# Performance work log

Measured on AMD Instinct MI355X. Metric: run time of the kernel, lower is better.

Reference implementation:

```python
import jax, jax.numpy as jnp
import numpy as np

H = 16         # heads
DH = 64        # dim_head
IMG = 32       # image_size (axial axis=0, along height)
SEQ_LEN = 1279 # seq_len
DIM = 1024
SCALE = DH ** -0.5


def setup_inputs() -> dict:
    key = jax.random.key(0)
    k1, k2, k3 = jax.random.split(key, 3)
    x = jax.random.normal(k1, (16, SEQ_LEN, DIM), dtype=jnp.float32)
    w_qkv = jax.random.normal(k2, (3 * H * DH, DIM), dtype=jnp.float32) * 0.02
    w_out = jax.random.normal(k3, (DIM, H * DH), dtype=jnp.float32) * 0.02
    b_out = jnp.zeros((DIM,), dtype=jnp.float32)
    return {"x": x, "w_qkv": w_qkv, "w_out": w_out, "b_out": b_out}


def reference(x, w_qkv, w_out, b_out):
    b, n, _ = x.shape
    img_seq = IMG * IMG                  # 1024
    text_len = SEQ_LEN + 1 - img_seq     # 256
    padding = SEQ_LEN - n + 1
    xp = jnp.pad(x, ((0, 0), (0, padding), (0, 0)))  # [b, seq_len+1, dim]

    qkv = xp @ w_qkv.T                   # [b, N, 3*H*DH]
    q, k, v = jnp.split(qkv, 3, axis=-1)

    def to_heads(t):
        B, N, _ = t.shape
        return t.reshape(B, N, H, DH).transpose(0, 2, 1, 3).reshape(B * H, N, DH)

    q, k, v = map(to_heads, (q, k, v))   # [(b h), N, DH]
    q = q * SCALE

    q_t, q_i = q[:, :-img_seq], q[:, -img_seq:]
    k_t, k_i = k[:, :-img_seq], k[:, -img_seq:]
    v_t, v_i = v[:, :-img_seq], v[:, -img_seq:]

    # ---- text self-attention (causal) ----
    dots_text = jnp.einsum('bid,bjd->bij', q_t, k_t)  # [(b h), T, T]
    mask_value = -jnp.finfo(dots_text.dtype).max
    T = text_len
    text_causal = jnp.triu(jnp.ones((T, T), dtype=bool), 1)
    dots_text = jnp.where(text_causal[None], mask_value, dots_text)
    attn_text = jax.nn.softmax(dots_text, axis=-1)
    out_text = jnp.einsum('bij,bjd->bid', attn_text, v_t)  # [(b h), T, DH]

    # ---- axial image attention (axis=0: attend along width within each row) ----
    qi = q_i.reshape(b * H, IMG, IMG, DH)  # b (h w) d -> b h w d
    ki = k_i.reshape(b * H, IMG, IMG, DH)
    vi = v_i.reshape(b * H, IMG, IMG, DH)

    dots_ii = jnp.einsum('bxid,bxjd->bxij', qi, ki)   # [(b h), IMG, IMG, IMG]
    dots_it = jnp.einsum('bxid,bjd->bxij', qi, k_t)   # [(b h), IMG, IMG, T]
    dots = jnp.concatenate((dots_it, dots_ii), axis=-1)  # [(b h), IMG, IMG, T+IMG]

    # text mask is all-valid (mask bool ones -> ~mask is all False); image part causal
    img_causal = jnp.triu(jnp.ones((IMG, IMG), dtype=bool), 1)
    full_mask = jnp.concatenate(
        (jnp.zeros((IMG, T), dtype=bool), img_causal), axis=-1)  # [IMG, T+IMG]
    dots = jnp.where(full_mask[None, None], mask_value, dots)

    attn = jax.nn.softmax(dots, axis=-1)
    a_it, a_ii = attn[..., :T], attn[..., T:]
    out_ii = jnp.einsum('bxij,bxjd->bxid', a_ii, vi)
    out_it = jnp.einsum('bxij,bjd->bxid', a_it, v_t)
    out_img = (out_ii + out_it).reshape(b * H, img_seq, DH)  # merge 'b x n d -> b (x n) d'

    out = jnp.concatenate((out_text, out_img), axis=1)       # [(b h), N, DH]
    N = out.shape[1]
    out = out.reshape(b, H, N, DH).transpose(0, 2, 1, 3).reshape(b, N, H * DH)
    out = out @ w_out.T + b_out
    return out[:, :n]
```

## Files before the change

kernel.cpp:

```cpp
#include <hip/hip_runtime.h>
#include <hip/hip_bf16.h>

typedef __hip_bfloat16 bf16;
using short8 = __attribute__((ext_vector_type(8))) short;
using f32x4  = __attribute__((ext_vector_type(4))) float;

#define MFMA16(a,b,c) __builtin_amdgcn_mfma_f32_16x16x32_bf16((a),(b),(c),0,0,0)

#define NB    16
#define SEQ   1280
#define NTOK  1279
#define DIMM  1024
#define NH    16
#define HD    64
#define TEXTLEN 256

__device__ __forceinline__ void gload_lds(const bf16* g, bf16* l) {
  __builtin_amdgcn_global_load_lds((const __attribute__((address_space(1))) void*)g,
                                   (__attribute__((address_space(3))) void*)l, 16, 0, 0);
}

__device__ __forceinline__ unsigned pk_bf16(float lo, float hi) {
  unsigned r;
  asm volatile("v_cvt_pk_bf16_f32 %0, %1, %2" : "=v"(r) : "v"(lo), "v"(hi));
  return r;
}

__global__ __launch_bounds__(256) void cvt_x_kernel(const float* __restrict__ x,
                                                    bf16* __restrict__ xb) {
  long idx = (long)blockIdx.x * 256 + threadIdx.x;
  long e = idx * 4;
  int bt = (int)(e >> 10);
  int c  = (int)(e & 1023);
  int b  = bt / SEQ;
  int t  = bt - b * SEQ;
  float4 v = make_float4(0.f, 0.f, 0.f, 0.f);
  if (t != NTOK) v = *(const float4*)(x + (size_t)(bt - b) * DIMM + c);
  union { bf16 h[4]; uint2 u; } p;
  p.h[0] = __float2bfloat16(v.x);
  p.h[1] = __float2bfloat16(v.y);
  p.h[2] = __float2bfloat16(v.z);
  p.h[3] = __float2bfloat16(v.w);
  *(uint2*)(xb + e) = p.u;
}

__global__ __launch_bounds__(256) void cvt_w_kernel(const float* __restrict__ w,
                                                    bf16* __restrict__ o) {
  long idx = (long)blockIdx.x * 256 + threadIdx.x;
  long e = idx * 4;
  float4 v = *(const float4*)(w + e);
  union { bf16 h[4]; uint2 u; } p;
  p.h[0] = __float2bfloat16(v.x);
  p.h[1] = __float2bfloat16(v.y);
  p.h[2] = __float2bfloat16(v.z);
  p.h[3] = __float2bfloat16(v.w);
  *(uint2*)(o + e) = p.u;
}

template<int MODE>
__global__ __launch_bounds__(256) void gemm_bt(
    const bf16* __restrict__ Ag, const bf16* __restrict__ Bg,
    bf16* __restrict__ O0, bf16* __restrict__ O1, bf16* __restrict__ O2,
    float* __restrict__ Of, const float* __restrict__ bias)
{
  constexpr int K = 1024;
  __shared__ bf16 As[128 * 32];
  __shared__ bf16 Bs[128 * 32];
  const int tid  = threadIdx.x;
  const int wave = tid >> 6;
  const int lane = tid & 63;
  const int l15  = lane & 15;
  const int l4   = lane >> 4;
  const int m0 = blockIdx.y * 128;
  const int n0 = blockIdx.x * 128;
  const int wr = wave >> 1, wc = wave & 1;

  f32x4 acc[4][4] = {};

  const int e0 = tid * 8;
  const int e1 = (256 + tid) * 8;
  const int r0 = e0 >> 5, c0 = e0 & 31;
  const int r1 = e1 >> 5, c1 = e1 & 31;
  bf16* ldsA0 = As + (wave * 64) * 8;
  bf16* ldsA1 = As + (256 + wave * 64) * 8;
  bf16* ldsB0 = Bs + (wave * 64) * 8;
  bf16* ldsB1 = Bs + (256 + wave * 64) * 8;
  const bf16* Abase = Ag + (size_t)m0 * K;
  const bf16* Bbase = Bg + (size_t)n0 * K;

  for (int k0 = 0; k0 < K; k0 += 32) {
    gload_lds(Abase + (size_t)r0 * K + k0 + c0, ldsA0);
    gload_lds(Abase + (size_t)r1 * K + k0 + c1, ldsA1);
    gload_lds(Bbase + (size_t)r0 * K + k0 + c0, ldsB0);
    gload_lds(Bbase + (size_t)r1 * K + k0 + c1, ldsB1);
    __syncthreads();
    short8 af[4], bf_[4];
#pragma unroll
    for (int i = 0; i < 4; ++i) {
      af[i]  = *(const short8*)(As + (wr * 64 + i * 16 + l15) * 32 + l4 * 8);
      bf_[i] = *(const short8*)(Bs + (wc * 64 + i * 16 + l15) * 32 + l4 * 8);
    }
#pragma unroll
    for (int mi = 0; mi < 4; ++mi)
#pragma unroll
      for (int ni = 0; ni < 4; ++ni)
        acc[mi][ni] = MFMA16(af[mi], bf_[ni], acc[mi][ni]);
    __syncthreads();
  }

  const int nb = n0 + wc * 64;
  const int b  = m0 / SEQ;
  const int tb = m0 - b * SEQ + wr * 64;

  if (MODE == 0) {
    const int which = n0 >> 10;
#pragma unroll
    for (int mi = 0; mi < 4; ++mi) {
#pragma unroll
      for (int ni = 0; ni < 4; ++ni) {
        const int n  = nb + ni * 16 + l15;
        const int h  = (n >> 6) & 15;
        const int d  = n & 63;
        const int bh = b * NH + h;
        const int t0 = tb + mi * 16 + l4 * 4;
        if (which == 2) {
          union { bf16 h4[4]; uint2 u; } p;
#pragma unroll
          for (int r = 0; r < 4; ++r) p.h4[r] = __float2bfloat16(acc[mi][ni][r]);
          *(uint2*)(O2 + (size_t)(bh * HD + d) * SEQ + t0) = p.u;
        } else {
          bf16* dst = (which == 0) ? O0 : O1;
          const float sc = (which == 0) ? 0.125f : 1.0f;
#pragma unroll
          for (int r = 0; r < 4; ++r)
            dst[((size_t)bh * SEQ + t0 + r) * HD + d] = __float2bfloat16(acc[mi][ni][r] * sc);
        }
      }
    }
  } else {
#pragma unroll
    for (int mi = 0; mi < 4; ++mi) {
#pragma unroll
      for (int ni = 0; ni < 4; ++ni) {
        const int n  = nb + ni * 16 + l15;
        const float bv = bias[n];
        const int t0 = tb + mi * 16 + l4 * 4;
#pragma unroll
        for (int r = 0; r < 4; ++r) {
          const int t = t0 + r;
          if (t < NTOK)
            Of[((size_t)b * NTOK + t) * DIMM + n] = acc[mi][ni][r] + bv;
        }
      }
    }
  }
}

__global__ __launch_bounds__(256, 3) void attn_kernel(
    const bf16* __restrict__ Qb, const bf16* __restrict__ Kb,
    const bf16* __restrict__ Vt, bf16* __restrict__ att)
{
  const int bidx = blockIdx.x;
  const int bh  = bidx / 10;
  const int sub = bidx - bh * 10;
  const int b = bh >> 4, h = bh & 15;
  const int wave = threadIdx.x >> 6;
  const int lane = threadIdx.x & 63;
  const int l15 = lane & 15, l4 = lane >> 4;

  const bf16* __restrict__ Qh = Qb + (size_t)bh * SEQ * HD;
  const bf16* __restrict__ Kh = Kb + (size_t)bh * SEQ * HD;
  const bf16* __restrict__ Vh = Vt + (size_t)bh * HD * SEQ;

  int q0, NT, isText;
  if (sub < 2) { const int c = sub * 4 + wave; q0 = c * 32; NT = (c >> 1) + 1; isText = 1; }
  else         { const int g = (sub - 2) * 4 + wave; q0 = TEXTLEN + g * 32; NT = 4; isText = 0; }

  short8 qf[2][2];
#pragma unroll
  for (int mi = 0; mi < 2; ++mi)
#pragma unroll
    for (int kb = 0; kb < 2; ++kb)
      qf[mi][kb] = *(const short8*)(Qh + (size_t)(q0 + mi * 16 + l15) * HD + kb * 32 + l4 * 8);

  f32x4 o[4][2] = {};
  float lsum[2] = {0.f, 0.f};

  for (int t = 0; t < NT; ++t) {
    const int kbase = t * 64;
    f32x4 s[2][4] = {};
#pragma unroll
    for (int ni = 0; ni < 4; ++ni) {
#pragma unroll
      for (int kb = 0; kb < 2; ++kb) {
        short8 kf = *(const short8*)(Kh + (size_t)(kbase + ni * 16 + l15) * HD + kb * 32 + l4 * 8);
#pragma unroll
        for (int mi = 0; mi < 2; ++mi)
          s[mi][ni] = MFMA16(kf, qf[mi][kb], s[mi][ni]);
      }
    }
    if (isText && t == NT - 1) {
#pragma unroll
      for (int mi = 0; mi < 2; ++mi)
#pragma unroll
        for (int ni = 0; ni < 4; ++ni)
#pragma unroll
          for (int r = 0; r < 4; ++r) {
            const int kk = kbase + ni * 16 + l4 * 4 + r;
            const int qq = q0 + mi * 16 + l15;
            if (kk > qq) s[mi][ni][r] = -1e30f;
          }
    }
    short8 pb[2][2];
#pragma unroll
    for (int mi = 0; mi < 2; ++mi) {
      float a0 = 0.f;
#pragma unroll
      for (int ni = 0; ni < 4; ++ni)
#pragma unroll
        for (int r = 0; r < 4; ++r) {
          const float e = __expf(s[mi][ni][r]);
          s[mi][ni][r] = e;
          a0 += e;
        }
      lsum[mi] += a0;
#pragma unroll
      for (int np = 0; np < 2; ++np) {
        union { unsigned w[4]; short8 v; } u;
        u.w[0] = pk_bf16(s[mi][2 * np][0], s[mi][2 * np][1]);
        u.w[1] = pk_bf16(s[mi][2 * np][2], s[mi][2 * np][3]);
        u.w[2] = pk_bf16(s[mi][2 * np + 1][0], s[mi][2 * np + 1][1]);
        u.w[3] = pk_bf16(s[mi][2 * np + 1][2], s[mi][2 * np + 1][3]);
        pb[mi][np] = u.v;
      }
    }
#pragma unroll
    for (int np = 0; np < 2; ++np) {
      const int kg = kbase + np * 32;
#pragma unroll
      for (int dblk = 0; dblk < 4; ++dblk) {
        const bf16* vp = Vh + (size_t)(dblk * 16 + l15) * SEQ + kg + l4 * 4;
        uint2 v0 = *(const uint2*)(vp);
        uint2 v1 = *(const uint2*)(vp + 16);
        union { uint4 u; short8 v; } va;
        va.u = make_uint4(v0.x, v0.y, v1.x, v1.y);
#pragma unroll
        for (int mi = 0; mi < 2; ++mi)
          o[dblk][mi] = MFMA16(va.v, pb[mi][np], o[dblk][mi]);
      }
    }
  }

  if (!isText) {
    const int kbase = q0;
    f32x4 s[2][2] = {};
#pragma unroll
    for (int ni = 0; ni < 2; ++ni) {
#pragma unroll
      for (int kb = 0; kb < 2; ++kb) {
        short8 kf = *(const short8*)(Kh + (size_t)(kbase + ni * 16 + l15) * HD + kb * 32 + l4 * 8);
#pragma unroll
        for (int mi = 0; mi < 2; ++mi)
          s[mi][ni] = MFMA16(kf, qf[mi][kb], s[mi][ni]);
      }
    }
    short8 pb[2];
#pragma unroll
    for (int mi = 0; mi < 2; ++mi) {
      float a0 = 0.f;
#pragma unroll
      for (int ni = 0; ni < 2; ++ni)
#pragma unroll
        for (int r = 0; r < 4; ++r) {
          const int kk = ni * 16 + l4 * 4 + r;
          const int qq = mi * 16 + l15;
          float e = (kk > qq) ? 0.f : __expf(s[mi][ni][r]);
          s[mi][ni][r] = e;
          a0 += e;
        }
      lsum[mi] += a0;
      union { unsigned w[4]; short8 v; } u;
      u.w[0] = pk_bf16(s[mi][0][0], s[mi][0][1]);
      u.w[1] = pk_bf16(s[mi][0][2], s[mi][0][3]);
      u.w[2] = pk_bf16(s[mi][1][0], s[mi][1][1]);
      u.w[3] = pk_bf16(s[mi][1][2], s[mi][1][3]);
      pb[mi] = u.v;
    }
#pragma unroll
    for (int dblk = 0; dblk < 4; ++dblk) {
      const bf16* vp = Vh + (size_t)(dblk * 16 + l15) * SEQ + kbase + l4 * 4;
      uint2 v0 = *(const uint2*)(vp);
      uint2 v1 = *(const uint2*)(vp + 16);
      union { uint4 u; short8 v; } va;
      va.u = make_uint4(v0.x, v0.y, v1.x, v1.y);
#pragma unroll
      for (int mi = 0; mi < 2; ++mi)
        o[dblk][mi] = MFMA16(va.v, pb[mi], o[dblk][mi]);
    }
  }

#pragma unroll
  for (int mi = 0; mi < 2; ++mi) {
    float l = lsum[mi];
    l += __shfl_xor(l, 16, 64);
    l += __shfl_xor(l, 32, 64);
    lsum[mi] = 1.0f / l;
  }
  bf16* ob = att + ((size_t)b * SEQ) * DIMM + h * HD;
#pragma unroll
  for (int dblk = 0; dblk < 4; ++dblk)
#pragma unroll
    for (int mi = 0; mi < 2; ++mi) {
      union { unsigned w[2]; uint2 u; } pk2;
      pk2.w[0] = pk_bf16(o[dblk][mi][0] * lsum[mi], o[dblk][mi][1] * lsum[mi]);
      pk2.w[1] = pk_bf16(o[dblk][mi][2] * lsum[mi], o[dblk][mi][3] * lsum[mi]);
      *(uint2*)(ob + (size_t)(q0 + mi * 16 + l15) * DIMM + dblk * 16 + l4 * 4) = pk2.u;
    }
}

extern "C" void kernel_launch(void* const* d_in, const int* in_sizes, int n_in,
                              void* d_out, int out_size, void* d_ws, size_t ws_size,
                              hipStream_t stream) {
  (void)in_sizes; (void)n_in; (void)out_size; (void)ws_size;
  const float* x     = (const float*)d_in[0];
  const float* w_qkv = (const float*)d_in[1];
  const float* w_out = (const float*)d_in[2];
  const float* b_out = (const float*)d_in[3];
  float* out = (float*)d_out;
  char* ws = (char*)d_ws;

  bf16* xb    = (bf16*)(ws);
  bf16* wqkvb = (bf16*)(ws + 41943040);
  bf16* woutb = (bf16*)(ws + 48234496);
  bf16* Qb    = (bf16*)(ws + 50331648);
  bf16* Kb    = (bf16*)(ws + 92274688);
  bf16* Vt    = (bf16*)(ws + 134217728);
  bf16* att   = xb;

  cvt_x_kernel<<<20480, 256, 0, stream>>>(x, xb);
  cvt_w_kernel<<<3072, 256, 0, stream>>>(w_qkv, wqkvb);
  cvt_w_kernel<<<1024, 256, 0, stream>>>(w_out, woutb);
  gemm_bt<0><<<dim3(24, 160), 256, 0, stream>>>(xb, wqkvb, Qb, Kb, Vt, nullptr, nullptr);
  attn_kernel<<<2560, 256, 0, stream>>>(Qb, Kb, Vt, att);
  gemm_bt<1><<<dim3(8, 160), 256, 0, stream>>>(att, woutb, nullptr, nullptr, nullptr, out, b_out);
}
```

Before: 530.7 us.

## Double-buffer K tiles in attention and remap GEMM workgroups across XCDs

```diff
diff --git a/kernel.cpp b/kernel.cpp
--- a/kernel.cpp
+++ b/kernel.cpp
@@ -57,7 +57,7 @@
   *(uint2*)(o + e) = p.u;
 }
 
-template<int MODE>
+template<int MODE, int NX, int NWG>
 __global__ __launch_bounds__(256) void gemm_bt(
     const bf16* __restrict__ Ag, const bf16* __restrict__ Bg,
     bf16* __restrict__ O0, bf16* __restrict__ O1, bf16* __restrict__ O2,
@@ -71,8 +71,11 @@
   const int lane = tid & 63;
   const int l15  = lane & 15;
   const int l4   = lane >> 4;
-  const int m0 = blockIdx.y * 128;
-  const int n0 = blockIdx.x * 128;
+
+  int w = blockIdx.y * NX + blockIdx.x;
+  w = (w & 7) * (NWG >> 3) + (w >> 3);
+  const int m0 = (w / NX) * 128;
+  const int n0 = (w % NX) * 128;
   const int wr = wave >> 1, wc = wave & 1;
 
   f32x4 acc[4][4] = {};
@@ -156,7 +159,104 @@
   }
 }
 
-__global__ __launch_bounds__(256, 3) void attn_kernel(
+__device__ __forceinline__ void load_ktile(const bf16* __restrict__ Kh, int kbase,
+                                           int l15, int l4, short8 (&buf)[8]) {
+#pragma unroll
+  for (int ni = 0; ni < 4; ++ni)
+#pragma unroll
+    for (int kb = 0; kb < 2; ++kb)
+      buf[ni * 2 + kb] = *(const short8*)(Kh + (size_t)(kbase + ni * 16 + l15) * HD + kb * 32 + l4 * 8);
+}
+
+__device__ __forceinline__ void load_kax(const bf16* __restrict__ Kh, int kbase,
+                                         int l15, int l4, short8 (&buf)[8]) {
+#pragma unroll
+  for (int ni = 0; ni < 2; ++ni)
+#pragma unroll
+    for (int kb = 0; kb < 2; ++kb)
+      buf[ni * 2 + kb] = *(const short8*)(Kh + (size_t)(kbase + ni * 16 + l15) * HD + kb * 32 + l4 * 8);
+}
+
+__device__ __forceinline__ void attn_tile(
+    const short8 (&kf)[8], short8 (&knxt)[8],
+    const short8 (&qf)[2][2],
+    const bf16* __restrict__ Kh, const bf16* __restrict__ Vh,
+    int kbase, int q0, int l15, int l4,
+    int pfmode, int pfbase, bool domask,
+    f32x4 (&o)[4][2], float (&lsum)[2])
+{
+  uint2 vv[16];
+#pragma unroll
+  for (int np = 0; np < 2; ++np)
+#pragma unroll
+    for (int dblk = 0; dblk < 4; ++dblk) {
+      const bf16* vp = Vh + (size_t)(dblk * 16 + l15) * SEQ + kbase + np * 32 + l4 * 4;
+      vv[np * 8 + dblk * 2]     = *(const uint2*)(vp);
+      vv[np * 8 + dblk * 2 + 1] = *(const uint2*)(vp + 16);
+    }
+
+  f32x4 s[2][4] = {};
+#pragma unroll
+  for (int ni = 0; ni < 4; ++ni)
+#pragma unroll
+    for (int kb = 0; kb < 2; ++kb)
+#pragma unroll
+      for (int mi = 0; mi < 2; ++mi)
+        s[mi][ni] = MFMA16(kf[ni * 2 + kb], qf[mi][kb], s[mi][ni]);
+
+  if (pfmode == 1)      load_ktile(Kh, pfbase, l15, l4, knxt);
+  else if (pfmode == 2) load_kax(Kh, pfbase, l15, l4, knxt);
+
+  if (domask) {
+#pragma unroll
+    for (int mi = 0; mi < 2; ++mi)
+#pragma unroll
+      for (int ni = 0; ni < 4; ++ni)
+#pragma unroll
+        for (int r = 0; r < 4; ++r) {
+          const int kk = kbase + ni * 16 + l4 * 4 + r;
+          const int qq = q0 + mi * 16 + l15;
+          if (kk > qq) s[mi][ni][r] = -1e30f;
+        }
+  }
+
+  short8 pb[2][2];
+#pragma unroll
+  for (int mi = 0; mi < 2; ++mi) {
+    float a0 = 0.f;
+#pragma unroll
+    for (int ni = 0; ni < 4; ++ni)
+#pragma unroll
+      for (int r = 0; r < 4; ++r) {
+        const float e = __expf(s[mi][ni][r]);
+        s[mi][ni][r] = e;
+        a0 += e;
+      }
+    lsum[mi] += a0;
+#pragma unroll
+    for (int np = 0; np < 2; ++np) {
+      union { unsigned w[4]; short8 v; } u;
+      u.w[0] = pk_bf16(s[mi][2 * np][0], s[mi][2 * np][1]);
+      u.w[1] = pk_bf16(s[mi][2 * np][2], s[mi][2 * np][3]);
+      u.w[2] = pk_bf16(s[mi][2 * np + 1][0], s[mi][2 * np + 1][1]);
+      u.w[3] = pk_bf16(s[mi][2 * np + 1][2], s[mi][2 * np + 1][3]);
+      pb[mi][np] = u.v;
+    }
+  }
+#pragma unroll
+  for (int np = 0; np < 2; ++np)
+#pragma unroll
+    for (int dblk = 0; dblk < 4; ++dblk) {
+      union { uint4 u; short8 v; } va;
+      va.u = make_uint4(vv[np * 8 + dblk * 2].x, vv[np * 8 + dblk * 2].y,
+                        vv[np * 8 + dblk * 2 + 1].x, vv[np * 8 + dblk * 2 + 1].y);
+#pragma unroll
+      for (int mi = 0; mi < 2; ++mi)
+        o[dblk][mi] = MFMA16(va.v, pb[mi][np], o[dblk][mi]);
+    }
+}
+
+__global__ __launch_bounds__(256, 2) void attn_kernel(
     const bf16* __restrict__ Qb, const bf16* __restrict__ Kb,
     const bf16* __restrict__ Vt, bf16* __restrict__ att)
 {
@@ -186,84 +286,45 @@
   f32x4 o[4][2] = {};
   float lsum[2] = {0.f, 0.f};
 
-  for (int t = 0; t < NT; ++t) {
-    const int kbase = t * 64;
-    f32x4 s[2][4] = {};
-#pragma unroll
-    for (int ni = 0; ni < 4; ++ni) {
-#pragma unroll
-      for (int kb = 0; kb < 2; ++kb) {
-        short8 kf = *(const short8*)(Kh + (size_t)(kbase + ni * 16 + l15) * HD + kb * 32 + l4 * 8);
-#pragma unroll
-        for (int mi = 0; mi < 2; ++mi)
-          s[mi][ni] = MFMA16(kf, qf[mi][kb], s[mi][ni]);
-      }
-    }
-    if (isText && t == NT - 1) {
-#pragma unroll
-      for (int mi = 0; mi < 2; ++mi)
-#pragma unroll
-        for (int ni = 0; ni < 4; ++ni)
-#pragma unroll
-          for (int r = 0; r < 4; ++r) {
-            const int kk = kbase + ni * 16 + l4 * 4 + r;
-            const int qq = q0 + mi * 16 + l15;
-            if (kk > qq) s[mi][ni][r] = -1e30f;
-          }
-    }
-    short8 pb[2][2];
-#pragma unroll
-    for (int mi = 0; mi < 2; ++mi) {
-      float a0 = 0.f;
-#pragma unroll
-      for (int ni = 0; ni < 4; ++ni)
-#pragma unroll
-        for (int r = 0; r < 4; ++r) {
-          const float e = __expf(s[mi][ni][r]);
-          s[mi][ni][r] = e;
-          a0 += e;
-        }
-      lsum[mi] += a0;
-#pragma unroll
-      for (int np = 0; np < 2; ++np) {
-        union { unsigned w[4]; short8 v; } u;
-        u.w[0] = pk_bf16(s[mi][2 * np][0], s[mi][2 * np][1]);
-        u.w[1] = pk_bf16(s[mi][2 * np][2], s[mi][2 * np][3]);
-        u.w[2] = pk_bf16(s[mi][2 * np + 1][0], s[mi][2 * np + 1][1]);
-        u.w[3] = pk_bf16(s[mi][2 * np + 1][2], s[mi][2 * np + 1][3]);
-        pb[mi][np] = u.v;
-      }
-    }
-#pragma unroll
-    for (int np = 0; np < 2; ++np) {
-      const int kg = kbase + np * 32;
-#pragma unroll
-      for (int dblk = 0; dblk < 4; ++dblk) {
-        const bf16* vp = Vh + (size_t)(dblk * 16 + l15) * SEQ + kg + l4 * 4;
-        uint2 v0 = *(const uint2*)(vp);
-        uint2 v1 = *(const uint2*)(vp + 16);
-        union { uint4 u; short8 v; } va;
-        va.u = make_uint4(v0.x, v0.y, v1.x, v1.y);
-#pragma unroll
-        for (int mi = 0; mi < 2; ++mi)
-          o[dblk][mi] = MFMA16(va.v, pb[mi][np], o[dblk][mi]);
-      }
-    }
+  short8 kA[8], kB[8];
+  load_ktile(Kh, 0, l15, l4, kA);
+
+  int t = 0;
+  while (t < NT) {
+    {
+      const int pfm = (t + 1 < NT) ? 1 : (isText ? 0 : 2);
+      const int pfb = (t + 1 < NT) ? (t + 1) * 64 : q0;
+      attn_tile(kA, kB, qf, Kh, Vh, t * 64, q0, l15, l4,
+                pfm, pfb, isText && (t == NT - 1), o, lsum);
+    }
+    ++t;
+    if (t >= NT) break;
+    {
+      const int pfm = (t + 1 < NT) ? 1 : (isText ? 0 : 2);
+      const int pfb = (t + 1 < NT) ? (t + 1) * 64 : q0;
+      attn_tile(kB, kA, qf, Kh, Vh, t * 64, q0, l15, l4,
+                pfm, pfb, isText && (t == NT - 1), o, lsum);
+    }
+    ++t;
   }
 
   if (!isText) {
     const int kbase = q0;
+    uint2 vv[8];
+#pragma unroll
+    for (int dblk = 0; dblk < 4; ++dblk) {
+      const bf16* vp = Vh + (size_t)(dblk * 16 + l15) * SEQ + kbase + l4 * 4;
+      vv[dblk * 2]     = *(const uint2*)(vp);
+      vv[dblk * 2 + 1] = *(const uint2*)(vp + 16);
+    }
     f32x4 s[2][2] = {};
 #pragma unroll
-    for (int ni = 0; ni < 2; ++ni) {
-#pragma unroll
-      for (int kb = 0; kb < 2; ++kb) {
-        short8 kf = *(const short8*)(Kh + (size_t)(kbase + ni * 16 + l15) * HD + kb * 32 + l4 * 8);
+    for (int ni = 0; ni < 2; ++ni)
+#pragma unroll
+      for (int kb = 0; kb < 2; ++kb)
 #pragma unroll
         for (int mi = 0; mi < 2; ++mi)
-          s[mi][ni] = MFMA16(kf, qf[mi][kb], s[mi][ni]);
-      }
-    }
+          s[mi][ni] = MFMA16(kA[ni * 2 + kb], qf[mi][kb], s[mi][ni]);
     short8 pb[2];
 #pragma unroll
     for (int mi = 0; mi < 2; ++mi) {
@@ -288,11 +349,8 @@
     }
 #pragma unroll
     for (int dblk = 0; dblk < 4; ++dblk) {
-      const bf16* vp = Vh + (size_t)(dblk * 16 + l15) * SEQ + kbase + l4 * 4;
-      uint2 v0 = *(const uint2*)(vp);
-      uint2 v1 = *(const uint2*)(vp + 16);
       union { uint4 u; short8 v; } va;
-      va.u = make_uint4(v0.x, v0.y, v1.x, v1.y);
+      va.u = make_uint4(vv[dblk * 2].x, vv[dblk * 2].y, vv[dblk * 2 + 1].x, vv[dblk * 2 + 1].y);
 #pragma unroll
       for (int mi = 0; mi < 2; ++mi)
         o[dblk][mi] = MFMA16(va.v, pb[mi], o[dblk][mi]);
@@ -340,7 +398,7 @@
   cvt_x_kernel<<<20480, 256, 0, stream>>>(x, xb);
   cvt_w_kernel<<<3072, 256, 0, stream>>>(w_qkv, wqkvb);
   cvt_w_kernel<<<1024, 256, 0, stream>>>(w_out, woutb);
-  gemm_bt<0><<<dim3(24, 160), 256, 0, stream>>>(xb, wqkvb, Qb, Kb, Vt, nullptr, nullptr);
+  gemm_bt<0, 24, 3840><<<dim3(24, 160), 256, 0, stream>>>(xb, wqkvb, Qb, Kb, Vt, nullptr, nullptr);
   attn_kernel<<<2560, 256, 0, stream>>>(Qb, Kb, Vt, att);
-  gemm_bt<1><<<dim3(8, 160), 256, 0, stream>>>(att, woutb, nullptr, nullptr, nullptr, out, b_out);
-}
+  gemm_bt<1, 8, 1280><<<dim3(8, 160), 256, 0, stream>>>(att, woutb, nullptr, nullptr, nullptr, out, b_out);
+}
```

After: 536.4 us. Within noise of the previous version (+1.1%).
